# Kernel tuning notes

Measured on AMD Instinct MI355X. Metric: run time of the kernel, lower is better.

The kernel has to match this reference:

```python
import jax, jax.numpy as jnp
import numpy as np

N = 50000      # num nodes
E = 800000     # num edges (before self loops)
DIN = 128      # input_dim
HID = 32       # hidden_dim per head
HEADS = 4
DOUT = 128     # output_dim
NEG_SLOPE = 0.2
EPS = 1e-5


def setup_inputs() -> dict:
    key = jax.random.key(0)
    ks = jax.random.split(key, 16)
    s = 0.05
    return {
        "x": jax.random.normal(ks[0], (N, DIN), dtype=jnp.float32),
        "edge_index": jax.random.randint(ks[1], (2, E), 0, N, dtype=jnp.int64),
        # GAT layer 1 (heads=4, concat=True)
        "W1": jax.random.normal(ks[2], (DIN, HEADS * HID), dtype=jnp.float32) * s,
        "att_src1": jax.random.normal(ks[3], (HEADS, HID), dtype=jnp.float32) * s,
        "att_dst1": jax.random.normal(ks[4], (HEADS, HID), dtype=jnp.float32) * s,
        "b1": jnp.zeros((HEADS * HID,), dtype=jnp.float32),
        # GAT layer 2 (heads=1, concat=False)
        "W2": jax.random.normal(ks[5], (HEADS * HID, DOUT), dtype=jnp.float32) * s,
        "att_src2": jax.random.normal(ks[6], (1, DOUT), dtype=jnp.float32) * s,
        "att_dst2": jax.random.normal(ks[7], (1, DOUT), dtype=jnp.float32) * s,
        "b2": jnp.zeros((DOUT,), dtype=jnp.float32),
        # LayerNorms
        "g1": jnp.ones((HEADS * HID,), dtype=jnp.float32),
        "be1": jnp.zeros((HEADS * HID,), dtype=jnp.float32),
        "g2": jnp.ones((DOUT,), dtype=jnp.float32),
        "be2": jnp.zeros((DOUT,), dtype=jnp.float32),
    }


def gat_conv(x, src, dst, W, a_src, a_dst, n_nodes):
    # x: [N, Fin]; W: [Fin, H*C]; a_src/a_dst: [H, C]
    H, C = a_src.shape
    h = (x @ W).reshape(-1, H, C)                       # [N, H, C]
    es = jnp.einsum("nhc,hc->nh", h, a_src)             # [N, H]
    ed = jnp.einsum("nhc,hc->nh", h, a_dst)             # [N, H]
    e = jax.nn.leaky_relu(es[src] + ed[dst], NEG_SLOPE)  # [E, H]
    # segment softmax over incoming edges of each dst node
    m = jax.ops.segment_max(e, dst, num_segments=n_nodes)
    a = jnp.exp(e - jax.lax.stop_gradient(m)[dst])
    den = jax.ops.segment_sum(a, dst, num_segments=n_nodes)
    alpha = a / den[dst]                                 # [E, H]
    out = jax.ops.segment_sum(alpha[:, :, None] * h[src], dst,
                              num_segments=n_nodes)      # [N, H, C]
    return out


def layer_norm(x, g, b):
    mu = jnp.mean(x, axis=-1, keepdims=True)
    var = jnp.mean((x - mu) ** 2, axis=-1, keepdims=True)
    return (x - mu) * jax.lax.rsqrt(var + EPS) * g + b


def reference(x, edge_index, W1, att_src1, att_dst1, b1,
              W2, att_src2, att_dst2, b2, g1, be1, g2, be2):
    n = x.shape[0]
    loop = jnp.arange(n, dtype=edge_index.dtype)
    src = jnp.concatenate([edge_index[0], loop])  # PyG add_self_loops=True
    dst = jnp.concatenate([edge_index[1], loop])

    h = gat_conv(x, src, dst, W1, att_src1, att_dst1, n)   # [N, 4, 32]
    h = h.reshape(n, -1) + b1                              # concat=True
    h = jax.nn.relu(layer_norm(h, g1, be1))                # dropout = id (eval)

    o = gat_conv(h, src, dst, W2, att_src2, att_dst2, n)   # [N, 1, DOUT]
    o = o[:, 0, :] + b2                                    # concat=False, 1 head
    o = jax.nn.relu(layer_norm(o, g2, be2))
    return o
```

## Files before the change

kernel.cpp:

```cpp
#include <hip/hip_runtime.h>

#define NEG 0.2f
#define LNEPS 1e-5f
#define BCAP 5120

static __device__ __forceinline__ float leaky(float e){ return fmaxf(e, NEG*e); }

static __device__ __forceinline__ unsigned pack_bf16(float a, float b){
  unsigned ua = __float_as_uint(a), ub = __float_as_uint(b);
  ua += 0x7FFFu + ((ua>>16)&1u);
  ub += 0x7FFFu + ((ub>>16)&1u);
  return (ua>>16) | (ub & 0xFFFF0000u);
}
static __device__ __forceinline__ float lo_bf(unsigned u){ return __uint_as_float(u<<16); }
static __device__ __forceinline__ float hi_bf(unsigned u){ return __uint_as_float(u & 0xFFFF0000u); }

typedef float f32x4 __attribute__((ext_vector_type(4)));
typedef short s16x8 __attribute__((ext_vector_type(8)));
union U4V8 { uint4 u; s16x8 v; };

static __device__ __forceinline__ void acc8(float w, uint4 u, float* a){
  a[0] = fmaf(w, lo_bf(u.x), a[0]);
  a[1] = fmaf(w, hi_bf(u.x), a[1]);
  a[2] = fmaf(w, lo_bf(u.y), a[2]);
  a[3] = fmaf(w, hi_bf(u.y), a[3]);
  a[4] = fmaf(w, lo_bf(u.z), a[4]);
  a[5] = fmaf(w, hi_bf(u.z), a[5]);
  a[6] = fmaf(w, lo_bf(u.w), a[6]);
  a[7] = fmaf(w, hi_bf(u.w), a[7]);
}

static __device__ __forceinline__ void wave_scan256(int* sm, int t){
  if (t < 64){
    int a0=sm[t*4], a1=sm[t*4+1], a2=sm[t*4+2], a3=sm[t*4+3];
    int s = a0+a1+a2+a3, sc = s;
    #pragma unroll
    for (int o=1;o<64;o<<=1){ int x = __shfl_up(sc, o); if (t >= o) sc += x; }
    int e = sc - s;
    sm[t*4]   = e;
    sm[t*4+1] = e + a0;
    sm[t*4+2] = e + a0 + a1;
    sm[t*4+3] = e + a0 + a1 + a2;
  }
}


static __device__ __forceinline__ void wprep_body(int i, const float* __restrict__ W1,
                                                  const float* __restrict__ W2,
                                                  uint4* __restrict__ W1b, uint4* __restrict__ W2b){
  const float* W = (i < 2048) ? W1 : W2;
  uint4* Wb = (i < 2048) ? W1b : W2b;
  int ii = i & 2047;
  int lane = ii & 63, t = (ii>>6)&7, k0 = ii>>9;
  int c = lane & 15, q = lane >> 4;
  const float* base = &W[(size_t)(k0*32 + q*8)*128 + t*16 + c];
  uint4 u;
  u.x = pack_bf16(base[0*128], base[1*128]);
  u.y = pack_bf16(base[2*128], base[3*128]);
  u.z = pack_bf16(base[4*128], base[5*128]);
  u.w = pack_bf16(base[6*128], base[7*128]);
  Wb[ii] = u;
}

static __device__ void bstage_body(int bb, const int* __restrict__ src, const int* __restrict__ dst,
                                   int* __restrict__ bfill, unsigned* __restrict__ stage, int E){
  __shared__ int h[256];
  __shared__ int sm[256];
  __shared__ int sb[256];
  __shared__ int cur[256];
  __shared__ int rb[256];
  __shared__ unsigned buf[2048];
  int t = threadIdx.x;
  h[t] = 0; __syncthreads();
  int base = bb * 2048;
  int cnt = min(2048, E - base);
  for (int i = t; i < cnt; i += 256) atomicAdd(&h[((unsigned)dst[base+i]) >> 8], 1);
  __syncthreads();
  int hv = h[t];
  sm[t] = hv; __syncthreads();
  wave_scan256(sm, t);
  __syncthreads();
  int excl = sm[t];
  sb[t] = excl;
  cur[t] = excl;
  rb[t] = (hv > 0) ? atomicAdd(&bfill[t], hv) : 0;
  __syncthreads();
  for (int i = t; i < cnt; i += 256){
    unsigned d = (unsigned)dst[base+i];
    unsigned v = (unsigned)src[base+i] | (d << 16);
    int p = atomicAdd(&cur[d >> 8], 1);
    buf[p] = v;
  }
  __syncthreads();
  for (int i = t; i < cnt; i += 256){
    unsigned v = buf[i];
    int b = v >> 24;
    int slot = rb[b] + (i - sb[b]);
    if (slot < BCAP) stage[(size_t)b*BCAP + slot] = v;
  }
}

static __device__ void bucket_body(int b, const unsigned* __restrict__ stage, const int* __restrict__ bfill,
                                   int* __restrict__ offA, int* __restrict__ offB,
                                   unsigned* __restrict__ csr2, int N){
  __shared__ int cnt[256];
  __shared__ int sm[256];
  __shared__ int cur[256];
  int t = threadIdx.x;
  int lo = b * BCAP;
  int hi = lo + min(bfill[b], BCAP);
  cnt[t] = 0; __syncthreads();
  for (int i = lo + t; i < hi; i += 256) atomicAdd(&cnt[(stage[i] >> 16) & 0xFF], 1);
  __syncthreads();
  sm[t] = cnt[t]; __syncthreads();
  wave_scan256(sm, t);
  __syncthreads();
  int ex = sm[t];
  cur[t] = ex;
  int d = (b << 8) + t;
  if (d < N){ offA[d] = lo + ex; offB[d] = lo + ex + cnt[t]; }
  __syncthreads();
  for (int i = lo + t; i < hi; i += 256){
    unsigned v = stage[i];
    int p = atomicAdd(&cur[(v >> 16) & 0xFF], 1);
    csr2[(size_t)(lo + p)] = v;
  }
}

template<int HEADS, bool PACKED>
static __device__ void gemm_body(int bid, const float* __restrict__ A, const unsigned* __restrict__ Ab,
                                 const uint4* __restrict__ Wb,
                                 const float* __restrict__ as, const float* __restrict__ ad,
                                 unsigned* __restrict__ Hb, float* __restrict__ es,
                                 float* __restrict__ ed, float* __restrict__ m0, int n){
  __shared__ unsigned hstage[4][16*68];
  int tid = threadIdx.x;
  int wave = tid >> 6, lane = tid & 63;
  int c = lane & 15, q = lane >> 4;
  int r0 = bid*64 + wave*16;
  int rowa = r0 + c;
  int rowc = min(rowa, n-1);
  f32x4 acc[8];
  #pragma unroll
  for (int t=0;t<8;++t) acc[t] = (f32x4){0.f,0.f,0.f,0.f};

  #pragma unroll
  for (int k0 = 0; k0 < 4; ++k0){
    U4V8 af;
    if (PACKED){
      af.u = *(const uint4*)&Ab[(size_t)rowc*64 + k0*16 + q*4];
    } else {
      const float* ap = &A[(size_t)rowc*128 + k0*32 + q*8];
      float4 v0 = *(const float4*)ap;
      float4 v1 = *(const float4*)(ap+4);
      af.u.x = pack_bf16(v0.x, v0.y);
      af.u.y = pack_bf16(v0.z, v0.w);
      af.u.z = pack_bf16(v1.x, v1.y);
      af.u.w = pack_bf16(v1.z, v1.w);
    }
    #pragma unroll
    for (int t=0;t<8;++t){
      U4V8 bf;
      bf.u = Wb[(k0*8+t)*64 + lane];
      acc[t] = __builtin_amdgcn_mfma_f32_16x16x32_bf16(af.v, bf.v, acc[t], 0, 0, 0);
    }
  }

  float asv[8], adv[8];
  #pragma unroll
  for (int t=0;t<8;++t){ asv[t] = as[t*16+c]; adv[t] = ad[t*16+c]; }
  if (HEADS == 4){
    float pes[4][4], ped[4][4];
    #pragma unroll
    for (int r=0;r<4;++r)
      #pragma unroll
      for (int h=0;h<4;++h){ pes[r][h]=0.f; ped[r][h]=0.f; }
    #pragma unroll
    for (int t=0;t<8;++t)
      #pragma unroll
      for (int r=0;r<4;++r){
        pes[r][t>>1] = fmaf(acc[t][r], asv[t], pes[r][t>>1]);
        ped[r][t>>1] = fmaf(acc[t][r], adv[t], ped[r][t>>1]);
      }
    #pragma unroll
    for (int r=0;r<4;++r)
      #pragma unroll
      for (int h=0;h<4;++h){
        #pragma unroll
        for (int m=1;m<16;m<<=1){
          pes[r][h] += __shfl_xor(pes[r][h], m);
          ped[r][h] += __shfl_xor(ped[r][h], m);
        }
      }
    if (c == 0){
      #pragma unroll
      for (int r=0;r<4;++r){
        int row2 = r0 + q*4 + r;
        if (row2 < n){
          float4 e = make_float4(pes[r][0],pes[r][1],pes[r][2],pes[r][3]);
          float4 d = make_float4(ped[r][0],ped[r][1],ped[r][2],ped[r][3]);
          float4 mm = make_float4(leaky(e.x+d.x),leaky(e.y+d.y),leaky(e.z+d.z),leaky(e.w+d.w));
          *(float4*)&es[(size_t)row2*4] = e;
          *(float4*)&ed[(size_t)row2*4] = d;
          *(float4*)&m0[(size_t)row2*4] = mm;
        }
      }
    }
  } else {
    float pes[4] = {0.f,0.f,0.f,0.f}, ped[4] = {0.f,0.f,0.f,0.f};
    #pragma unroll
    for (int t=0;t<8;++t)
      #pragma unroll
      for (int r=0;r<4;++r){
        pes[r] = fmaf(acc[t][r], asv[t], pes[r]);
        ped[r] = fmaf(acc[t][r], adv[t], ped[r]);
      }
    #pragma unroll
    for (int r=0;r<4;++r){
      #pragma unroll
      for (int m=1;m<16;m<<=1){
        pes[r] += __shfl_xor(pes[r], m);
        ped[r] += __shfl_xor(ped[r], m);
      }
    }
    if (c == 0){
      #pragma unroll
      for (int r=0;r<4;++r){
        int row2 = r0 + q*4 + r;
        if (row2 < n){
          es[row2] = pes[r]; ed[row2] = ped[r]; m0[row2] = leaky(pes[r]+ped[r]);
        }
      }
    }
  }

  unsigned* hs = hstage[wave];
  #pragma unroll
  for (int t=0;t<8;++t)
    #pragma unroll
    for (int r=0;r<4;++r){
      float other = __shfl_xor(acc[t][r], 1);
      if (!(c & 1)) hs[(q*4+r)*68 + t*8 + (c>>1)] = pack_bf16(acc[t][r], other);
    }
  #pragma unroll
  for (int it=0; it<4; ++it){
    int idx = it*64 + lane;
    int rr = idx >> 4, c4 = idx & 15;
    int grow = r0 + rr;
    if (grow < n)
      *(uint4*)&Hb[(size_t)grow*64 + c4*4] = *(uint4*)&hs[rr*68 + c4*4];
  }
}


__global__ __launch_bounds__(256) void k_A(const float* __restrict__ W1, const float* __restrict__ W2,
                                           uint4* __restrict__ W1b, uint4* __restrict__ W2b,
                                           const int* __restrict__ src, const int* __restrict__ dst,
                                           int* __restrict__ bfill, unsigned* __restrict__ stage, int E){
  int bid = blockIdx.x;
  if (bid < 16){
    wprep_body(bid*256 + threadIdx.x, W1, W2, W1b, W2b);
  } else {
    bstage_body(bid - 16, src, dst, bfill, stage, E);
  }
}

__global__ __launch_bounds__(256) void k_B(const float* __restrict__ x, const uint4* __restrict__ W1b,
                                           const float* __restrict__ as1, const float* __restrict__ ad1,
                                           unsigned* __restrict__ Hb, float* __restrict__ es1,
                                           float* __restrict__ ed1, float* __restrict__ m01,
                                           const unsigned* __restrict__ stage, const int* __restrict__ bfill,
                                           int* __restrict__ offA, int* __restrict__ offB,
                                           unsigned* __restrict__ csr2, int N, int gb){
  int bid = blockIdx.x;
  if (bid < gb){
    gemm_body<4,false>(bid, x, nullptr, W1b, as1, ad1, Hb, es1, ed1, m01, N);
  } else {
    bucket_body(bid - gb, stage, bfill, offA, offB, csr2, N);
  }
}

template<int HEADS, bool PACKED>
__global__ __launch_bounds__(256) void k_gemm_mfma(const float* __restrict__ A,
                                                   const unsigned* __restrict__ Ab,
                                                   const uint4* __restrict__ Wb,
                                                   const float* __restrict__ as, const float* __restrict__ ad,
                                                   unsigned* __restrict__ Hb, float* __restrict__ es,
                                                   float* __restrict__ ed, float* __restrict__ m0, int n){
  gemm_body<HEADS,PACKED>(blockIdx.x, A, Ab, Wb, as, ad, Hb, es, ed, m0, n);
}


template<bool OUT_PACKED>
__global__ __launch_bounds__(256) void k_agg4(const unsigned* __restrict__ Hb,
                                              const float* __restrict__ es, const float* __restrict__ ed,
                                              const float* __restrict__ m0,
                                              const int* __restrict__ offA, const int* __restrict__ offB,
                                              const unsigned* __restrict__ csr2,
                                              const float* __restrict__ bias, const float* __restrict__ g,
                                              const float* __restrict__ be, float* __restrict__ out,
                                              unsigned* __restrict__ outp, int N){
  int lane = threadIdx.x & 63;
  int node = blockIdx.x*4 + (threadIdx.x >> 6);
  if (node >= N) return;
  int grp = lane >> 4;
  int fi  = lane & 15;
  int hsrc = (fi >> 2) << 4;
  float edn = ed[(size_t)node*4 + grp];
  float m0n = m0[(size_t)node*4 + grp];
  float a[8];
  #pragma unroll
  for (int k=0;k<8;++k) a[k] = 0.f;
  float l = 0.f;
  int j0 = offA[node], j1 = offB[node];
  for (int c0 = j0; c0 < j1; c0 += 16){
    int m = j1 - c0;
    int sv = 0; float wv = 0.f;
    if (fi < m){
      unsigned v = csr2[c0 + fi];
      sv = v & 0xFFFF;
      wv = __expf(leaky(es[(size_t)sv*4 + grp] + edn) - m0n);
    }
    int   s0 = __shfl(sv, grp),          s1 = __shfl(sv, 4 + grp),
          s2 = __shfl(sv, 8 + grp),      s3 = __shfl(sv, 12 + grp);
    float w0 = __shfl(wv, hsrc + grp),   w1 = __shfl(wv, hsrc + 4 + grp),
          w2 = __shfl(wv, hsrc + 8 + grp), w3 = __shfl(wv, hsrc + 12 + grp);
    uint4 u0 = *(const uint4*)&Hb[(size_t)s0*64 + fi*4];
    uint4 u1 = *(const uint4*)&Hb[(size_t)s1*64 + fi*4];
    uint4 u2 = *(const uint4*)&Hb[(size_t)s2*64 + fi*4];
    uint4 u3 = *(const uint4*)&Hb[(size_t)s3*64 + fi*4];
    l += ((w0 + w1) + (w2 + w3));
    acc8(w0, u0, a);
    acc8(w1, u1, a);
    acc8(w2, u2, a);
    acc8(w3, u3, a);
  }
  #pragma unroll
  for (int k=0;k<8;++k){
    a[k] += __shfl_xor(a[k], 16);
    a[k] += __shfl_xor(a[k], 32);
  }
  l += __shfl_xor(l, 16);
  l += __shfl_xor(l, 32);
  uint4 us = *(const uint4*)&Hb[(size_t)node*64 + fi*4];
  a[0] += lo_bf(us.x); a[1] += hi_bf(us.x);
  a[2] += lo_bf(us.y); a[3] += hi_bf(us.y);
  a[4] += lo_bf(us.z); a[5] += hi_bf(us.z);
  a[6] += lo_bf(us.w); a[7] += hi_bf(us.w);
  l += 1.f;

  float rl = __frcp_rn(l);
  float4 bv0 = *(const float4*)&bias[fi*8];
  float4 bv1 = *(const float4*)&bias[fi*8 + 4];
  float v[8];
  v[0] = a[0]*rl + bv0.x; v[1] = a[1]*rl + bv0.y;
  v[2] = a[2]*rl + bv0.z; v[3] = a[3]*rl + bv0.w;
  v[4] = a[4]*rl + bv1.x; v[5] = a[5]*rl + bv1.y;
  v[6] = a[6]*rl + bv1.z; v[7] = a[7]*rl + bv1.w;
  float s = ((v[0]+v[1])+(v[2]+v[3])) + ((v[4]+v[5])+(v[6]+v[7]));
  #pragma unroll
  for (int mm=1; mm<16; mm<<=1) s += __shfl_xor(s, mm);
  float mu = s * (1.f/128.f);
  float d[8], ss = 0.f;
  #pragma unroll
  for (int k=0;k<8;++k){ d[k] = v[k]-mu; ss += d[k]*d[k]; }
  #pragma unroll
  for (int mm=1; mm<16; mm<<=1) ss += __shfl_xor(ss, mm);
  float rs = rsqrtf(ss*(1.f/128.f) + LNEPS);
  float4 gv0 = *(const float4*)&g[fi*8];
  float4 gv1 = *(const float4*)&g[fi*8 + 4];
  float4 ev0 = *(const float4*)&be[fi*8];
  float4 ev1 = *(const float4*)&be[fi*8 + 4];
  float y[8];
  y[0] = fmaxf(d[0]*rs*gv0.x + ev0.x, 0.f);
  y[1] = fmaxf(d[1]*rs*gv0.y + ev0.y, 0.f);
  y[2] = fmaxf(d[2]*rs*gv0.z + ev0.z, 0.f);
  y[3] = fmaxf(d[3]*rs*gv0.w + ev0.w, 0.f);
  y[4] = fmaxf(d[4]*rs*gv1.x + ev1.x, 0.f);
  y[5] = fmaxf(d[5]*rs*gv1.y + ev1.y, 0.f);
  y[6] = fmaxf(d[6]*rs*gv1.z + ev1.z, 0.f);
  y[7] = fmaxf(d[7]*rs*gv1.w + ev1.w, 0.f);
  if (grp == 0){
    if (OUT_PACKED){
      uint4 o;
      o.x = pack_bf16(y[0], y[1]);
      o.y = pack_bf16(y[2], y[3]);
      o.z = pack_bf16(y[4], y[5]);
      o.w = pack_bf16(y[6], y[7]);
      *(uint4*)&outp[(size_t)node*64 + fi*4] = o;
    } else {
      *(float4*)&out[(size_t)node*128 + fi*8]     = make_float4(y[0],y[1],y[2],y[3]);
      *(float4*)&out[(size_t)node*128 + fi*8 + 4] = make_float4(y[4],y[5],y[6],y[7]);
    }
  }
}

__global__ __launch_bounds__(256) void k_agg1(const unsigned* __restrict__ Hb,
                                              const float* __restrict__ es, const float* __restrict__ ed,
                                              const float* __restrict__ m0,
                                              const int* __restrict__ offA, const int* __restrict__ offB,
                                              const unsigned* __restrict__ csr2,
                                              const float* __restrict__ bias, const float* __restrict__ g,
                                              const float* __restrict__ be, float* __restrict__ out, int N){
  int lane = threadIdx.x & 63;
  int node = blockIdx.x*4 + (threadIdx.x >> 6);
  if (node >= N) return;
  int grp = lane >> 4;
  int fi  = lane & 15;
  float edn = ed[node];
  float m0n = m0[node];
  float a[8];
  #pragma unroll
  for (int k=0;k<8;++k) a[k] = 0.f;
  float l = 0.f;
  int j0 = offA[node], j1 = offB[node];
  for (int c0 = j0; c0 < j1; c0 += 64){
    int m = min(64, j1 - c0);
    int sv = 0; float wv = 0.f;
    if (lane < m){
      unsigned v = csr2[c0 + lane];
      sv = v & 0xFFFF;
      wv = __expf(leaky(es[sv] + edn) - m0n);
    }
    for (int jj = 0; jj < m; jj += 16){
      int   s0 = __shfl(sv, jj + grp),      s1 = __shfl(sv, jj + 4 + grp),
            s2 = __shfl(sv, jj + 8 + grp),  s3 = __shfl(sv, jj + 12 + grp);
      float w0 = __shfl(wv, jj + grp),      w1 = __shfl(wv, jj + 4 + grp),
            w2 = __shfl(wv, jj + 8 + grp),  w3 = __shfl(wv, jj + 12 + grp);
      uint4 u0 = *(const uint4*)&Hb[(size_t)s0*64 + fi*4];
      uint4 u1 = *(const uint4*)&Hb[(size_t)s1*64 + fi*4];
      uint4 u2 = *(const uint4*)&Hb[(size_t)s2*64 + fi*4];
      uint4 u3 = *(const uint4*)&Hb[(size_t)s3*64 + fi*4];
      l += ((w0 + w1) + (w2 + w3));
      acc8(w0, u0, a);
      acc8(w1, u1, a);
      acc8(w2, u2, a);
      acc8(w3, u3, a);
    }
  }
  #pragma unroll
  for (int k=0;k<8;++k){
    a[k] += __shfl_xor(a[k], 16);
    a[k] += __shfl_xor(a[k], 32);
  }
  l += __shfl_xor(l, 16);
  l += __shfl_xor(l, 32);
  uint4 us = *(const uint4*)&Hb[(size_t)node*64 + fi*4];
  a[0] += lo_bf(us.x); a[1] += hi_bf(us.x);
  a[2] += lo_bf(us.y); a[3] += hi_bf(us.y);
  a[4] += lo_bf(us.z); a[5] += hi_bf(us.z);
  a[6] += lo_bf(us.w); a[7] += hi_bf(us.w);
  l += 1.f;

  float rl = __frcp_rn(l);
  float4 bv0 = *(const float4*)&bias[fi*8];
  float4 bv1 = *(const float4*)&bias[fi*8 + 4];
  float v[8];
  v[0] = a[0]*rl + bv0.x; v[1] = a[1]*rl + bv0.y;
  v[2] = a[2]*rl + bv0.z; v[3] = a[3]*rl + bv0.w;
  v[4] = a[4]*rl + bv1.x; v[5] = a[5]*rl + bv1.y;
  v[6] = a[6]*rl + bv1.z; v[7] = a[7]*rl + bv1.w;
  float s = ((v[0]+v[1])+(v[2]+v[3])) + ((v[4]+v[5])+(v[6]+v[7]));
  #pragma unroll
  for (int mm=1; mm<16; mm<<=1) s += __shfl_xor(s, mm);
  float mu = s * (1.f/128.f);
  float d[8], ss = 0.f;
  #pragma unroll
  for (int k=0;k<8;++k){ d[k] = v[k]-mu; ss += d[k]*d[k]; }
  #pragma unroll
  for (int mm=1; mm<16; mm<<=1) ss += __shfl_xor(ss, mm);
  float rs = rsqrtf(ss*(1.f/128.f) + LNEPS);
  float4 gv0 = *(const float4*)&g[fi*8];
  float4 gv1 = *(const float4*)&g[fi*8 + 4];
  float4 ev0 = *(const float4*)&be[fi*8];
  float4 ev1 = *(const float4*)&be[fi*8 + 4];
  float y[8];
  y[0] = fmaxf(d[0]*rs*gv0.x + ev0.x, 0.f);
  y[1] = fmaxf(d[1]*rs*gv0.y + ev0.y, 0.f);
  y[2] = fmaxf(d[2]*rs*gv0.z + ev0.z, 0.f);
  y[3] = fmaxf(d[3]*rs*gv0.w + ev0.w, 0.f);
  y[4] = fmaxf(d[4]*rs*gv1.x + ev1.x, 0.f);
  y[5] = fmaxf(d[5]*rs*gv1.y + ev1.y, 0.f);
  y[6] = fmaxf(d[6]*rs*gv1.z + ev1.z, 0.f);
  y[7] = fmaxf(d[7]*rs*gv1.w + ev1.w, 0.f);
  if (grp == 0){
    *(float4*)&out[(size_t)node*128 + fi*8]     = make_float4(y[0],y[1],y[2],y[3]);
    *(float4*)&out[(size_t)node*128 + fi*8 + 4] = make_float4(y[4],y[5],y[6],y[7]);
  }
}


extern "C" void kernel_launch(void* const* d_in, const int* in_sizes, int n_in,
                              void* d_out, int out_size, void* d_ws, size_t ws_size,
                              hipStream_t stream){
  const float* x   = (const float*)d_in[0];
  const int*   ei  = (const int*)  d_in[1];
  const float* W1  = (const float*)d_in[2];
  const float* as1 = (const float*)d_in[3];
  const float* ad1 = (const float*)d_in[4];
  const float* b1  = (const float*)d_in[5];
  const float* W2  = (const float*)d_in[6];
  const float* as2 = (const float*)d_in[7];
  const float* ad2 = (const float*)d_in[8];
  const float* b2  = (const float*)d_in[9];
  const float* g1  = (const float*)d_in[10];
  const float* be1 = (const float*)d_in[11];
  const float* g2  = (const float*)d_in[12];
  const float* be2 = (const float*)d_in[13];

  int N = in_sizes[0] / 128;
  int E = in_sizes[1] / 2;
  const int* src = ei;
  const int* dst = ei + E;

  int NB = (N + 255) >> 8;

  char* p = (char*)d_ws;
  auto carve = [&](size_t bytes)->char*{ char* r = p; p += ((bytes + 255) / 256) * 256; return r; };
  unsigned* Hb = (unsigned*)carve((size_t)N*64*4);
  unsigned* Bb = (unsigned*)carve((size_t)N*64*4);
  float* es1 = (float*)carve((size_t)N*4*4);
  float* ed1 = (float*)carve((size_t)N*4*4);
  float* m01 = (float*)carve((size_t)N*4*4);
  float* es2 = (float*)carve((size_t)N*4);
  float* ed2 = (float*)carve((size_t)N*4);
  float* m02 = (float*)carve((size_t)N*4);
  int* offA  = (int*)carve((size_t)N*4);
  int* offB  = (int*)carve((size_t)N*4);
  unsigned* stg  = (unsigned*)carve((size_t)NB*BCAP*4);
  unsigned* csr2 = (unsigned*)carve((size_t)NB*BCAP*4);
  uint4* W1b = (uint4*)carve(2048*16);
  uint4* W2b = (uint4*)carve(2048*16);
  int* bfill = (int*)carve(256*4);

  hipMemsetAsync(bfill, 0, 1024, stream);

  int nbe = (E + 2047) / 2048;
  int gb  = (N + 63) / 64;
  int nb4 = (N + 3) / 4;

  k_A<<<16 + nbe, 256, 0, stream>>>(W1, W2, W1b, W2b, src, dst, bfill, stg, E);
  k_B<<<gb + NB, 256, 0, stream>>>(x, W1b, as1, ad1, Hb, es1, ed1, m01,
                                   stg, bfill, offA, offB, csr2, N, gb);
  k_agg4<true><<<nb4, 256, 0, stream>>>(Hb, es1, ed1, m01, offA, offB, csr2,
                                        b1, g1, be1, nullptr, Bb, N);
  k_gemm_mfma<1,true><<<gb, 256, 0, stream>>>(nullptr, Bb, W2b, as2, ad2, Hb, es2, ed2, m02, N);
  k_agg1<<<nb4, 256, 0, stream>>>(Hb, es2, ed2, m02, offA, offB, csr2,
                                  b2, g2, be2, (float*)d_out, N);
}
```

Measured before the change: 223.5 us.

## Fuse all stages into one persistent cooperative kernel with grid syncs

```diff
diff --git a/kernel.cpp b/kernel.cpp
--- a/kernel.cpp
+++ b/kernel.cpp
@@ -1,4 +1,7 @@
 #include <hip/hip_runtime.h>
+#include <hip/hip_cooperative_groups.h>
+
+namespace cg = cooperative_groups;
 
 #define NEG 0.2f
 #define LNEPS 1e-5f
@@ -63,13 +66,14 @@
 }
 
 static __device__ void bstage_body(int bb, const int* __restrict__ src, const int* __restrict__ dst,
-                                   int* __restrict__ bfill, unsigned* __restrict__ stage, int E){
-  __shared__ int h[256];
-  __shared__ int sm[256];
-  __shared__ int sb[256];
-  __shared__ int cur[256];
-  __shared__ int rb[256];
-  __shared__ unsigned buf[2048];
+                                   int* __restrict__ bfill, unsigned* __restrict__ stage, int E,
+                                   char* smem){
+  int* h   = (int*)(smem);
+  int* sm  = (int*)(smem + 1024);
+  int* sb  = (int*)(smem + 2048);
+  int* cur = (int*)(smem + 3072);
+  int* rb  = (int*)(smem + 4096);
+  unsigned* buf = (unsigned*)(smem + 5120);
   int t = threadIdx.x;
   h[t] = 0; __syncthreads();
   int base = bb * 2048;
@@ -101,11 +105,11 @@
 }
 
 static __device__ void bucket_body(int b, const unsigned* __restrict__ stage, const int* __restrict__ bfill,
-                                   int* __restrict__ offA, int* __restrict__ offB,
-                                   unsigned* __restrict__ csr2, int N){
-  __shared__ int cnt[256];
-  __shared__ int sm[256];
-  __shared__ int cur[256];
+                                   int2* __restrict__ offs, unsigned* __restrict__ csr2, int N,
+                                   char* smem){
+  int* cnt = (int*)(smem);
+  int* sm  = (int*)(smem + 1024);
+  int* cur = (int*)(smem + 2048);
   int t = threadIdx.x;
   int lo = b * BCAP;
   int hi = lo + min(bfill[b], BCAP);
@@ -118,7 +122,7 @@
   int ex = sm[t];
   cur[t] = ex;
   int d = (b << 8) + t;
-  if (d < N){ offA[d] = lo + ex; offB[d] = lo + ex + cnt[t]; }
+  if (d < N) offs[d] = make_int2(lo + ex, lo + ex + cnt[t]);
   __syncthreads();
   for (int i = lo + t; i < hi; i += 256){
     unsigned v = stage[i];
@@ -132,8 +136,8 @@
                                  const uint4* __restrict__ Wb,
                                  const float* __restrict__ as, const float* __restrict__ ad,
                                  unsigned* __restrict__ Hb, float* __restrict__ es,
-                                 float* __restrict__ ed, float* __restrict__ m0, int n){
-  __shared__ unsigned hstage[4][16*68];
+                                 float* __restrict__ ed, float* __restrict__ m0, int n,
+                                 unsigned* hstage){
   int tid = threadIdx.x;
   int wave = tid >> 6, lane = tid & 63;
   int c = lane & 15, q = lane >> 4;
@@ -234,7 +238,7 @@
     }
   }
 
-  unsigned* hs = hstage[wave];
+  unsigned* hs = hstage + wave*(16*68);
   #pragma unroll
   for (int t=0;t<8;++t)
     #pragma unroll
@@ -253,87 +257,53 @@
 }
 
 
-__global__ __launch_bounds__(256) void k_A(const float* __restrict__ W1, const float* __restrict__ W2,
-                                           uint4* __restrict__ W1b, uint4* __restrict__ W2b,
-                                           const int* __restrict__ src, const int* __restrict__ dst,
-                                           int* __restrict__ bfill, unsigned* __restrict__ stage, int E){
-  int bid = blockIdx.x;
-  if (bid < 16){
-    wprep_body(bid*256 + threadIdx.x, W1, W2, W1b, W2b);
-  } else {
-    bstage_body(bid - 16, src, dst, bfill, stage, E);
-  }
-}
-
-__global__ __launch_bounds__(256) void k_B(const float* __restrict__ x, const uint4* __restrict__ W1b,
-                                           const float* __restrict__ as1, const float* __restrict__ ad1,
-                                           unsigned* __restrict__ Hb, float* __restrict__ es1,
-                                           float* __restrict__ ed1, float* __restrict__ m01,
-                                           const unsigned* __restrict__ stage, const int* __restrict__ bfill,
-                                           int* __restrict__ offA, int* __restrict__ offB,
-                                           unsigned* __restrict__ csr2, int N, int gb){
-  int bid = blockIdx.x;
-  if (bid < gb){
-    gemm_body<4,false>(bid, x, nullptr, W1b, as1, ad1, Hb, es1, ed1, m01, N);
-  } else {
-    bucket_body(bid - gb, stage, bfill, offA, offB, csr2, N);
-  }
-}
-
-template<int HEADS, bool PACKED>
-__global__ __launch_bounds__(256) void k_gemm_mfma(const float* __restrict__ A,
-                                                   const unsigned* __restrict__ Ab,
-                                                   const uint4* __restrict__ Wb,
-                                                   const float* __restrict__ as, const float* __restrict__ ad,
-                                                   unsigned* __restrict__ Hb, float* __restrict__ es,
-                                                   float* __restrict__ ed, float* __restrict__ m0, int n){
-  gemm_body<HEADS,PACKED>(blockIdx.x, A, Ab, Wb, as, ad, Hb, es, ed, m0, n);
-}
-
-
-template<bool OUT_PACKED>
-__global__ __launch_bounds__(256) void k_agg4(const unsigned* __restrict__ Hb,
-                                              const float* __restrict__ es, const float* __restrict__ ed,
-                                              const float* __restrict__ m0,
-                                              const int* __restrict__ offA, const int* __restrict__ offB,
-                                              const unsigned* __restrict__ csr2,
-                                              const float* __restrict__ bias, const float* __restrict__ g,
-                                              const float* __restrict__ be, float* __restrict__ out,
-                                              unsigned* __restrict__ outp, int N){
+static __device__ void agg4_body(int u, const unsigned* __restrict__ Hb,
+                                 const float* __restrict__ es, const float* __restrict__ ed,
+                                 const float* __restrict__ m0,
+                                 const int2* __restrict__ offs, const unsigned* __restrict__ csr2,
+                                 const float* __restrict__ bias, const float* __restrict__ g,
+                                 const float* __restrict__ be, unsigned* __restrict__ outp, int N){
   int lane = threadIdx.x & 63;
-  int node = blockIdx.x*4 + (threadIdx.x >> 6);
+  int node = u*4 + (threadIdx.x >> 6);
   if (node >= N) return;
   int grp = lane >> 4;
   int fi  = lane & 15;
   int hsrc = (fi >> 2) << 4;
   float edn = ed[(size_t)node*4 + grp];
   float m0n = m0[(size_t)node*4 + grp];
+  int2 jj2 = offs[node];
+  int j0 = jj2.x, j1 = jj2.y;
+  uint4 us = *(const uint4*)&Hb[(size_t)node*64 + fi*4];
   float a[8];
   #pragma unroll
   for (int k=0;k<8;++k) a[k] = 0.f;
   float l = 0.f;
-  int j0 = offA[node], j1 = offB[node];
-  for (int c0 = j0; c0 < j1; c0 += 16){
+  for (int c0 = j0; c0 < j1; c0 += 64){
     int m = j1 - c0;
-    int sv = 0; float wv = 0.f;
-    if (fi < m){
-      unsigned v = csr2[c0 + fi];
-      sv = v & 0xFFFF;
-      wv = __expf(leaky(es[(size_t)sv*4 + grp] + edn) - m0n);
-    }
-    int   s0 = __shfl(sv, grp),          s1 = __shfl(sv, 4 + grp),
-          s2 = __shfl(sv, 8 + grp),      s3 = __shfl(sv, 12 + grp);
-    float w0 = __shfl(wv, hsrc + grp),   w1 = __shfl(wv, hsrc + 4 + grp),
-          w2 = __shfl(wv, hsrc + 8 + grp), w3 = __shfl(wv, hsrc + 12 + grp);
-    uint4 u0 = *(const uint4*)&Hb[(size_t)s0*64 + fi*4];
-    uint4 u1 = *(const uint4*)&Hb[(size_t)s1*64 + fi*4];
-    uint4 u2 = *(const uint4*)&Hb[(size_t)s2*64 + fi*4];
-    uint4 u3 = *(const uint4*)&Hb[(size_t)s3*64 + fi*4];
-    l += ((w0 + w1) + (w2 + w3));
-    acc8(w0, u0, a);
-    acc8(w1, u1, a);
-    acc8(w2, u2, a);
-    acc8(w3, u3, a);
+    int v = 0;
+    if (lane < m) v = (int)(csr2[c0 + lane] & 0xFFFFu);
+    #pragma unroll
+    for (int k = 0; k < 4; ++k){
+      int ke = k*16;
+      if (ke < m){
+        int svk = __shfl(v, ke + fi);
+        float wvk = 0.f;
+        if (ke + fi < m) wvk = __expf(leaky(es[(size_t)svk*4 + grp] + edn) - m0n);
+        int   s0 = __shfl(v, ke + grp),        s1 = __shfl(v, ke + 4 + grp);
+        int   s2 = __shfl(v, ke + 8 + grp),    s3 = __shfl(v, ke + 12 + grp);
+        float w0 = __shfl(wvk, hsrc + grp),    w1 = __shfl(wvk, hsrc + 4 + grp);
+        float w2 = __shfl(wvk, hsrc + 8 + grp),w3 = __shfl(wvk, hsrc + 12 + grp);
+        uint4 u0 = *(const uint4*)&Hb[(size_t)s0*64 + fi*4];
+        uint4 u1 = *(const uint4*)&Hb[(size_t)s1*64 + fi*4];
+        uint4 u2 = *(const uint4*)&Hb[(size_t)s2*64 + fi*4];
+        uint4 u3 = *(const uint4*)&Hb[(size_t)s3*64 + fi*4];
+        l += ((w0 + w1) + (w2 + w3));
+        acc8(w0, u0, a);
+        acc8(w1, u1, a);
+        acc8(w2, u2, a);
+        acc8(w3, u3, a);
+      }
+    }
   }
   #pragma unroll
   for (int k=0;k<8;++k){
@@ -342,7 +312,6 @@
   }
   l += __shfl_xor(l, 16);
   l += __shfl_xor(l, 32);
-  uint4 us = *(const uint4*)&Hb[(size_t)node*64 + fi*4];
   a[0] += lo_bf(us.x); a[1] += hi_bf(us.x);
   a[2] += lo_bf(us.y); a[3] += hi_bf(us.y);
   a[4] += lo_bf(us.z); a[5] += hi_bf(us.z);
@@ -381,61 +350,60 @@
   y[6] = fmaxf(d[6]*rs*gv1.z + ev1.z, 0.f);
   y[7] = fmaxf(d[7]*rs*gv1.w + ev1.w, 0.f);
   if (grp == 0){
-    if (OUT_PACKED){
-      uint4 o;
-      o.x = pack_bf16(y[0], y[1]);
-      o.y = pack_bf16(y[2], y[3]);
-      o.z = pack_bf16(y[4], y[5]);
-      o.w = pack_bf16(y[6], y[7]);
-      *(uint4*)&outp[(size_t)node*64 + fi*4] = o;
-    } else {
-      *(float4*)&out[(size_t)node*128 + fi*8]     = make_float4(y[0],y[1],y[2],y[3]);
-      *(float4*)&out[(size_t)node*128 + fi*8 + 4] = make_float4(y[4],y[5],y[6],y[7]);
-    }
-  }
-}
-
-__global__ __launch_bounds__(256) void k_agg1(const unsigned* __restrict__ Hb,
-                                              const float* __restrict__ es, const float* __restrict__ ed,
-                                              const float* __restrict__ m0,
-                                              const int* __restrict__ offA, const int* __restrict__ offB,
-                                              const unsigned* __restrict__ csr2,
-                                              const float* __restrict__ bias, const float* __restrict__ g,
-                                              const float* __restrict__ be, float* __restrict__ out, int N){
+    uint4 o;
+    o.x = pack_bf16(y[0], y[1]);
+    o.y = pack_bf16(y[2], y[3]);
+    o.z = pack_bf16(y[4], y[5]);
+    o.w = pack_bf16(y[6], y[7]);
+    *(uint4*)&outp[(size_t)node*64 + fi*4] = o;
+  }
+}
+
+static __device__ void agg1_body(int u, const unsigned* __restrict__ Hb,
+                                 const float* __restrict__ es, const float* __restrict__ ed,
+                                 const float* __restrict__ m0,
+                                 const int2* __restrict__ offs, const unsigned* __restrict__ csr2,
+                                 const float* __restrict__ bias, const float* __restrict__ g,
+                                 const float* __restrict__ be, float* __restrict__ out, int N){
   int lane = threadIdx.x & 63;
-  int node = blockIdx.x*4 + (threadIdx.x >> 6);
+  int node = u*4 + (threadIdx.x >> 6);
   if (node >= N) return;
   int grp = lane >> 4;
   int fi  = lane & 15;
   float edn = ed[node];
   float m0n = m0[node];
+  int2 jj2 = offs[node];
+  int j0 = jj2.x, j1 = jj2.y;
+  uint4 us = *(const uint4*)&Hb[(size_t)node*64 + fi*4];
   float a[8];
   #pragma unroll
   for (int k=0;k<8;++k) a[k] = 0.f;
   float l = 0.f;
-  int j0 = offA[node], j1 = offB[node];
   for (int c0 = j0; c0 < j1; c0 += 64){
-    int m = min(64, j1 - c0);
-    int sv = 0; float wv = 0.f;
+    int m = j1 - c0;
+    int v = 0; float wv = 0.f;
     if (lane < m){
-      unsigned v = csr2[c0 + lane];
-      sv = v & 0xFFFF;
-      wv = __expf(leaky(es[sv] + edn) - m0n);
-    }
-    for (int jj = 0; jj < m; jj += 16){
-      int   s0 = __shfl(sv, jj + grp),      s1 = __shfl(sv, jj + 4 + grp),
-            s2 = __shfl(sv, jj + 8 + grp),  s3 = __shfl(sv, jj + 12 + grp);
-      float w0 = __shfl(wv, jj + grp),      w1 = __shfl(wv, jj + 4 + grp),
-            w2 = __shfl(wv, jj + 8 + grp),  w3 = __shfl(wv, jj + 12 + grp);
-      uint4 u0 = *(const uint4*)&Hb[(size_t)s0*64 + fi*4];
-      uint4 u1 = *(const uint4*)&Hb[(size_t)s1*64 + fi*4];
-      uint4 u2 = *(const uint4*)&Hb[(size_t)s2*64 + fi*4];
-      uint4 u3 = *(const uint4*)&Hb[(size_t)s3*64 + fi*4];
-      l += ((w0 + w1) + (w2 + w3));
-      acc8(w0, u0, a);
-      acc8(w1, u1, a);
-      acc8(w2, u2, a);
-      acc8(w3, u3, a);
+      v = (int)(csr2[c0 + lane] & 0xFFFFu);
+      wv = __expf(leaky(es[v] + edn) - m0n);
+    }
+    #pragma unroll
+    for (int k = 0; k < 4; ++k){
+      int ke = k*16;
+      if (ke < m){
+        int   s0 = __shfl(v, ke + grp),      s1 = __shfl(v, ke + 4 + grp);
+        int   s2 = __shfl(v, ke + 8 + grp),  s3 = __shfl(v, ke + 12 + grp);
+        float w0 = __shfl(wv, ke + grp),     w1 = __shfl(wv, ke + 4 + grp);
+        float w2 = __shfl(wv, ke + 8 + grp), w3 = __shfl(wv, ke + 12 + grp);
+        uint4 u0 = *(const uint4*)&Hb[(size_t)s0*64 + fi*4];
+        uint4 u1 = *(const uint4*)&Hb[(size_t)s1*64 + fi*4];
+        uint4 u2 = *(const uint4*)&Hb[(size_t)s2*64 + fi*4];
+        uint4 u3 = *(const uint4*)&Hb[(size_t)s3*64 + fi*4];
+        l += ((w0 + w1) + (w2 + w3));
+        acc8(w0, u0, a);
+        acc8(w1, u1, a);
+        acc8(w2, u2, a);
+        acc8(w3, u3, a);
+      }
     }
   }
   #pragma unroll
@@ -445,7 +413,6 @@
   }
   l += __shfl_xor(l, 16);
   l += __shfl_xor(l, 32);
-  uint4 us = *(const uint4*)&Hb[(size_t)node*64 + fi*4];
   a[0] += lo_bf(us.x); a[1] += hi_bf(us.x);
   a[2] += lo_bf(us.y); a[3] += hi_bf(us.y);
   a[4] += lo_bf(us.z); a[5] += hi_bf(us.z);
@@ -455,18 +422,18 @@
   float rl = __frcp_rn(l);
   float4 bv0 = *(const float4*)&bias[fi*8];
   float4 bv1 = *(const float4*)&bias[fi*8 + 4];
-  float v[8];
-  v[0] = a[0]*rl + bv0.x; v[1] = a[1]*rl + bv0.y;
-  v[2] = a[2]*rl + bv0.z; v[3] = a[3]*rl + bv0.w;
-  v[4] = a[4]*rl + bv1.x; v[5] = a[5]*rl + bv1.y;
-  v[6] = a[6]*rl + bv1.z; v[7] = a[7]*rl + bv1.w;
-  float s = ((v[0]+v[1])+(v[2]+v[3])) + ((v[4]+v[5])+(v[6]+v[7]));
+  float v2[8];
+  v2[0] = a[0]*rl + bv0.x; v2[1] = a[1]*rl + bv0.y;
+  v2[2] = a[2]*rl + bv0.z; v2[3] = a[3]*rl + bv0.w;
+  v2[4] = a[4]*rl + bv1.x; v2[5] = a[5]*rl + bv1.y;
+  v2[6] = a[6]*rl + bv1.z; v2[7] = a[7]*rl + bv1.w;
+  float s = ((v2[0]+v2[1])+(v2[2]+v2[3])) + ((v2[4]+v2[5])+(v2[6]+v2[7]));
   #pragma unroll
   for (int mm=1; mm<16; mm<<=1) s += __shfl_xor(s, mm);
   float mu = s * (1.f/128.f);
   float d[8], ss = 0.f;
   #pragma unroll
-  for (int k=0;k<8;++k){ d[k] = v[k]-mu; ss += d[k]*d[k]; }
+  for (int k=0;k<8;++k){ d[k] = v2[k]-mu; ss += d[k]*d[k]; }
   #pragma unroll
   for (int mm=1; mm<16; mm<<=1) ss += __shfl_xor(ss, mm);
   float rs = rsqrtf(ss*(1.f/128.f) + LNEPS);
@@ -490,6 +457,63 @@
 }
 
 
+struct GParams {
+  const float *x; const int *src; const int *dst;
+  const float *W1, *as1, *ad1, *b1;
+  const float *W2, *as2, *ad2, *b2;
+  const float *g1, *be1, *g2, *be2;
+  unsigned *Hb, *Bb;
+  float *es1, *ed1, *m01, *es2, *ed2, *m02;
+  int2 *offs;
+  unsigned *stg, *csr2;
+  uint4 *W1b, *W2b;
+  int *bfill;
+  float *out;
+  int N, E, NB, gb, nb4, nbe;
+};
+
+__global__ __launch_bounds__(256, 4) void kfused(GParams p){
+  __shared__ __align__(16) char smem[17408];
+  cg::grid_group gg = cg::this_grid();
+  const int bid = blockIdx.x;
+  const int G = gridDim.x;
+  const int tid = threadIdx.x;
+
+  for (int u = bid; u < 16 + p.nbe; u += G){
+    if (u < 16) wprep_body(u*256 + tid, p.W1, p.W2, p.W1b, p.W2b);
+    else        bstage_body(u - 16, p.src, p.dst, p.bfill, p.stg, p.E, smem);
+    __syncthreads();
+  }
+  __threadfence();
+  gg.sync();
+
+  for (int u = bid; u < p.gb + p.NB; u += G){
+    if (u < p.gb) gemm_body<4,false>(u, p.x, nullptr, p.W1b, p.as1, p.ad1,
+                                     p.Hb, p.es1, p.ed1, p.m01, p.N, (unsigned*)smem);
+    else          bucket_body(u - p.gb, p.stg, p.bfill, p.offs, p.csr2, p.N, smem);
+    __syncthreads();
+  }
+  __threadfence();
+  gg.sync();
+
+  for (int u = bid; u < p.nb4; u += G)
+    agg4_body(u, p.Hb, p.es1, p.ed1, p.m01, p.offs, p.csr2, p.b1, p.g1, p.be1, p.Bb, p.N);
+  __threadfence();
+  gg.sync();
+
+  for (int u = bid; u < p.gb; u += G){
+    gemm_body<1,true>(u, nullptr, p.Bb, p.W2b, p.as2, p.ad2,
+                      p.Hb, p.es2, p.ed2, p.m02, p.N, (unsigned*)smem);
+    __syncthreads();
+  }
+  __threadfence();
+  gg.sync();
+
+  for (int u = bid; u < p.nb4; u += G)
+    agg1_body(u, p.Hb, p.es2, p.ed2, p.m02, p.offs, p.csr2, p.b2, p.g2, p.be2, p.out, p.N);
+}
+
+
 extern "C" void kernel_launch(void* const* d_in, const int* in_sizes, int n_in,
                               void* d_out, int out_size, void* d_ws, size_t ws_size,
                               hipStream_t stream){
@@ -525,8 +549,7 @@
   float* es2 = (float*)carve((size_t)N*4);
   float* ed2 = (float*)carve((size_t)N*4);
   float* m02 = (float*)carve((size_t)N*4);
-  int* offA  = (int*)carve((size_t)N*4);
-  int* offB  = (int*)carve((size_t)N*4);
+  int2* offs = (int2*)carve((size_t)N*8);
   unsigned* stg  = (unsigned*)carve((size_t)NB*BCAP*4);
   unsigned* csr2 = (unsigned*)carve((size_t)NB*BCAP*4);
   uint4* W1b = (uint4*)carve(2048*16);
@@ -535,16 +558,38 @@
 
   hipMemsetAsync(bfill, 0, 1024, stream);
 
-  int nbe = (E + 2047) / 2048;
-  int gb  = (N + 63) / 64;
-  int nb4 = (N + 3) / 4;
-
-  k_A<<<16 + nbe, 256, 0, stream>>>(W1, W2, W1b, W2b, src, dst, bfill, stg, E);
-  k_B<<<gb + NB, 256, 0, stream>>>(x, W1b, as1, ad1, Hb, es1, ed1, m01,
-                                   stg, bfill, offA, offB, csr2, N, gb);
-  k_agg4<true><<<nb4, 256, 0, stream>>>(Hb, es1, ed1, m01, offA, offB, csr2,
-                                        b1, g1, be1, nullptr, Bb, N);
-  k_gemm_mfma<1,true><<<gb, 256, 0, stream>>>(nullptr, Bb, W2b, as2, ad2, Hb, es2, ed2, m02, N);
-  k_agg1<<<nb4, 256, 0, stream>>>(Hb, es2, ed2, m02, offA, offB, csr2,
-                                  b2, g2, be2, (float*)d_out, N);
-}
+  GParams gp;
+  gp.x = x; gp.src = src; gp.dst = dst;
+  gp.W1 = W1; gp.as1 = as1; gp.ad1 = ad1; gp.b1 = b1;
+  gp.W2 = W2; gp.as2 = as2; gp.ad2 = ad2; gp.b2 = b2;
+  gp.g1 = g1; gp.be1 = be1; gp.g2 = g2; gp.be2 = be2;
+  gp.Hb = Hb; gp.Bb = Bb;
+  gp.es1 = es1; gp.ed1 = ed1; gp.m01 = m01;
+  gp.es2 = es2; gp.ed2 = ed2; gp.m02 = m02;
+  gp.offs = offs; gp.stg = stg; gp.csr2 = csr2;
+  gp.W1b = W1b; gp.W2b = W2b; gp.bfill = bfill;
+  gp.out = (float*)d_out;
+  gp.N = N; gp.E = E; gp.NB = NB;
+  gp.gb = (N + 63) / 64;
+  gp.nb4 = (N + 3) / 4;
+  gp.nbe = (E + 2047) / 2048;
+
+  static int gridBlocks = 0;
+  if (gridBlocks == 0){
+    int dev = 0; hipGetDevice(&dev);
+    hipDeviceProp_t prop{};
+    int ncu = 256;
+    if (hipGetDeviceProperties(&prop, dev) == hipSuccess && prop.multiProcessorCount > 0)
+      ncu = prop.multiProcessorCount;
+    int maxb = 0;
+    hipOccupancyMaxActiveBlocksPerMultiprocessor(&maxb, (const void*)kfused, 256, 0);
+    if (maxb < 1) maxb = 1;
+    long cap = (long)maxb * ncu;
+    if (cap > 2048) cap = 2048;
+    gridBlocks = (int)cap;
+  }
+
+  void* args[] = { (void*)&gp };
+  hipLaunchCooperativeKernel((const void*)kfused, dim3(gridBlocks), dim3(256),
+                             args, 0, stream);
+}
```

Result: slower. 795.2 us (+255.8%).
